# Performance work log

Hardware: AMD Instinct MI355X
Metric: run time of the kernel (lower is better)

## Reference

```python
import jax, jax.numpy as jnp
import numpy as np

GRID_SIZE = 64
THRESHOLD = 1.0
SIGMA = 1.5
K_SHARP = 2.0


def _gaussian_kernel(sigma):
    ksize = max(int(4 * sigma) | 1, 3)
    x = jnp.arange(ksize, dtype=jnp.float32) - ksize // 2
    g1d = jnp.exp(-x ** 2 / (2.0 * sigma ** 2))
    g2d = g1d[None, :] * g1d[:, None]
    g2d = g2d / g2d.sum()
    return g2d[None, None]  # (1,1,k,k) OIHW


def setup_inputs() -> dict:
    key = jax.random.key(0)
    k1, k2, k3, k4 = jax.random.split(key, 4)
    B, V, P, N, MAXP = 4, 512, 8192, 2000, 8
    positions = jax.random.uniform(k1, (B, V, 2), dtype=jnp.float32) * 2.0 - 1.0
    pin_offsets = jax.random.normal(k2, (P, 2), dtype=jnp.float32) * 0.05
    net_to_pin = jax.random.randint(k3, (N, MAXP), 0, P, dtype=jnp.int32)
    pin_to_macro = jax.random.randint(k4, (P,), 0, V, dtype=jnp.int32)
    return {"positions": positions, "pin_offsets": pin_offsets,
            "net_to_pin": net_to_pin, "pin_to_macro": pin_to_macro}


def reference(positions, pin_offsets, net_to_pin, pin_to_macro):
    B = positions.shape[0]
    M = GRID_SIZE
    num_nets = net_to_pin.shape[0]

    # pin positions: (B, P, 2) -- no rotation (rotation_onehot=None branch)
    pin_pos = positions[:, pin_to_macro, :] + pin_offsets[None]

    # per-net bounding boxes over valid pins
    valid = net_to_pin >= 0                                  # (N, maxp)
    safe_idx = jnp.maximum(net_to_pin, 0)
    net_pin_pos = pin_pos[:, safe_idx, :]                    # (B, N, maxp, 2)
    mask = valid[None, :, :, None]
    bbox_max = jnp.max(jnp.where(mask, net_pin_pos, -1e9), axis=2)  # (B, N, 2)
    bbox_min = jnp.min(jnp.where(mask, net_pin_pos, 1e9), axis=2)

    # to grid coordinates
    bbox_max_g = (bbox_max + 1.0) * 0.5 * (M - 1)
    bbox_min_g = (bbox_min + 1.0) * 0.5 * (M - 1)

    # soft rectangular indicators on the MxM grid
    gx = jnp.arange(M, dtype=jnp.float32)
    grid_x, grid_y = jnp.meshgrid(gx, gx, indexing="xy")     # (M, M)
    grid_x = grid_x[None, None]                               # (1,1,M,M)
    grid_y = grid_y[None, None]
    x_min = bbox_min_g[..., 0][..., None, None]               # (B,N,1,1)
    x_max = bbox_max_g[..., 0][..., None, None]
    y_min = bbox_min_g[..., 1][..., None, None]
    y_max = bbox_max_g[..., 1][..., None, None]

    in_x = jax.nn.sigmoid(K_SHARP * (grid_x - x_min + 0.5)) * \
           jax.nn.sigmoid(K_SHARP * (x_max - grid_x + 0.5))
    in_y = jax.nn.sigmoid(K_SHARP * (grid_y - y_min + 0.5)) * \
           jax.nn.sigmoid(K_SHARP * (y_max - grid_y + 0.5))
    indicator = in_x * in_y                                    # (B,N,M,M)

    bbox_size = jnp.maximum((x_max - x_min + 1.0) * (y_max - y_min + 1.0), 1.0)
    rudy = jnp.sum(indicator / bbox_size, axis=1, keepdims=True)  # (B,1,M,M)

    # gaussian smoothing (SAME padding)
    kernel = _gaussian_kernel(SIGMA)
    pad = kernel.shape[-1] // 2
    rudy_smooth = jax.lax.conv_general_dilated(
        rudy, kernel, window_strides=(1, 1),
        padding=((pad, pad), (pad, pad)),
        dimension_numbers=("NCHW", "OIHW", "NCHW"))

    overflow = jax.nn.relu(rudy_smooth - THRESHOLD)
    penalty = jnp.sum(overflow ** 2, axis=(1, 2, 3))           # (B,)
    return penalty, rudy_smooth
```

## Files before the change

kernel.cpp:

```cpp
#include <hip/hip_runtime.h>

#define GRID   64
#define CELLS  (GRID * GRID)
#define BATCH  4
#define NV     512
#define NNET   2000
#define MAXPIN 8
#define NB     32
#define NPART_MAX 63

__device__ __forceinline__ float sigmoidf_fast(float z) {
    return 1.0f / (1.0f + __expf(-z));
}

__global__ __launch_bounds__(256)
void rudy_partial_kernel(const float* __restrict__ positions,
                         const float* __restrict__ pin_offsets,
                         const int*   __restrict__ net_to_pin,
                         const int*   __restrict__ pin_to_macro,
                         float* __restrict__ partial,
                         int subs) {
    const int pb = blockIdx.x;
    const int b  = blockIdx.y;
    const int t  = threadIdx.x;

    __shared__ float s_inx[NB][GRID];
    __shared__ float s_iny[NB][GRID];
    __shared__ float s_xmin[NB], s_xmax[NB], s_ymin[NB], s_ymax[NB], s_inv[NB];

    const int lane = t & 63;
    const int w    = t >> 6;

    float acc[16];
    #pragma unroll
    for (int k = 0; k < 16; ++k) acc[k] = 0.0f;

    const int base = pb * subs * NB;

    for (int sub = 0; sub < subs; ++sub) {
        const int n0 = base + sub * NB;

        {
            const int nl = t >> 3;
            const int j  = t & 7;
            const int n  = n0 + nl;
            int pi = (n < NNET) ? net_to_pin[n * MAXPIN + j] : -1;
            int sp = pi > 0 ? pi : 0;
            int v  = pin_to_macro[sp];
            float px = positions[(b * NV + v) * 2 + 0] + pin_offsets[sp * 2 + 0];
            float py = positions[(b * NV + v) * 2 + 1] + pin_offsets[sp * 2 + 1];
            bool valid = pi >= 0;
            float xmx = valid ? px : -1e9f;
            float xmn = valid ? px :  1e9f;
            float ymx = valid ? py : -1e9f;
            float ymn = valid ? py :  1e9f;
            #pragma unroll
            for (int off = 1; off < 8; off <<= 1) {
                xmx = fmaxf(xmx, __shfl_xor(xmx, off, 64));
                xmn = fminf(xmn, __shfl_xor(xmn, off, 64));
                ymx = fmaxf(ymx, __shfl_xor(ymx, off, 64));
                ymn = fminf(ymn, __shfl_xor(ymn, off, 64));
            }
            if (j == 0) {
                float xming = (xmn + 1.0f) * 31.5f;
                float xmaxg = (xmx + 1.0f) * 31.5f;
                float yming = (ymn + 1.0f) * 31.5f;
                float ymaxg = (ymx + 1.0f) * 31.5f;
                float size = fmaxf((xmaxg - xming + 1.0f) * (ymaxg - yming + 1.0f), 1.0f);
                s_xmin[nl] = xming; s_xmax[nl] = xmaxg;
                s_ymin[nl] = yming; s_ymax[nl] = ymaxg;
                s_inv[nl]  = 1.0f / size;
            }
        }
        __syncthreads();

        #pragma unroll
        for (int i = 0; i < 16; ++i) {
            int vv    = i * 256 + t;
            int n     = vv >> 7;
            int rem   = vv & 127;
            int which = rem >> 6;
            int coord = rem & 63;
            float c  = (float)coord;
            float lo = which ? s_ymin[n] : s_xmin[n];
            float hi = which ? s_ymax[n] : s_xmax[n];
            float val = sigmoidf_fast(2.0f * (c - lo + 0.5f)) *
                        sigmoidf_fast(2.0f * (hi - c + 0.5f));
            if (which) s_iny[n][coord] = val;
            else       s_inx[n][coord] = val * s_inv[n];
        }
        __syncthreads();

        for (int n = 0; n < NB; ++n) {
            float xv = s_inx[n][lane];
            const float4* iny4 = (const float4*)&s_iny[n][w * 16];
            #pragma unroll
            for (int k4 = 0; k4 < 4; ++k4) {
                float4 yv = iny4[k4];
                acc[k4 * 4 + 0] += yv.x * xv;
                acc[k4 * 4 + 1] += yv.y * xv;
                acc[k4 * 4 + 2] += yv.z * xv;
                acc[k4 * 4 + 3] += yv.w * xv;
            }
        }
    }

    float* dst = partial + ((size_t)b * gridDim.x + pb) * CELLS;
    #pragma unroll
    for (int k = 0; k < 16; ++k)
        dst[(w * 16 + k) * GRID + lane] = acc[k];
}

__global__ __launch_bounds__(1024)
void reduce_smooth_kernel(const float* __restrict__ partial,
                          float* __restrict__ out_penalty,
                          float* __restrict__ out_smooth,
                          int npart) {
    const int b = blockIdx.x;
    const int t = threadIdx.x;

    __shared__ float tile[CELLS];
    __shared__ float tmp [CELLS];
    __shared__ float red [16];

    float g[7];
    {
        float s = 0.0f;
        #pragma unroll
        for (int i = 0; i < 7; ++i) {
            float d = (float)(i - 3);
            g[i] = expf(-d * d / 4.5f);
            s += g[i];
        }
        float inv = 1.0f / s;
        #pragma unroll
        for (int i = 0; i < 7; ++i) g[i] *= inv;
    }

    const float4* src = (const float4*)(partial + (size_t)b * npart * CELLS);
    float4 a = {0.0f, 0.0f, 0.0f, 0.0f};
    #pragma unroll 4
    for (int p = 0; p < npart; ++p) {
        float4 v = src[p * (CELLS / 4) + t];
        a.x += v.x; a.y += v.y; a.z += v.z; a.w += v.w;
    }
    ((float4*)tile)[t] = a;
    __syncthreads();

    #pragma unroll
    for (int i = 0; i < 4; ++i) {
        int c = i * 1024 + t;
        int y = c >> 6, x = c & 63;
        float s = 0.0f;
        #pragma unroll
        for (int d = -3; d <= 3; ++d) {
            int xx = x + d;
            if (xx >= 0 && xx < GRID) s += g[d + 3] * tile[y * GRID + xx];
        }
        tmp[c] = s;
    }
    __syncthreads();

    float local = 0.0f;
    #pragma unroll
    for (int i = 0; i < 4; ++i) {
        int c = i * 1024 + t;
        int y = c >> 6, x = c & 63;
        float s = 0.0f;
        #pragma unroll
        for (int d = -3; d <= 3; ++d) {
            int yy = y + d;
            if (yy >= 0 && yy < GRID) s += g[d + 3] * tmp[yy * GRID + x];
        }
        out_smooth[b * CELLS + c] = s;
        float ov = s - 1.0f;
        ov = ov > 0.0f ? ov : 0.0f;
        local += ov * ov;
    }

    #pragma unroll
    for (int off = 32; off > 0; off >>= 1) local += __shfl_down(local, off, 64);
    if ((t & 63) == 0) red[t >> 6] = local;
    __syncthreads();
    if (t == 0) {
        float s = 0.0f;
        #pragma unroll
        for (int i = 0; i < 16; ++i) s += red[i];
        out_penalty[b] = s;
    }
}

extern "C" void kernel_launch(void* const* d_in, const int* in_sizes, int n_in,
                              void* d_out, int out_size, void* d_ws, size_t ws_size,
                              hipStream_t stream) {
    const float* positions    = (const float*)d_in[0];
    const float* pin_offsets  = (const float*)d_in[1];
    const int*   net_to_pin   = (const int*)d_in[2];
    const int*   pin_to_macro = (const int*)d_in[3];
    float* out     = (float*)d_out;
    float* partial = (float*)d_ws;

    int npart = (int)(ws_size / ((size_t)BATCH * CELLS * sizeof(float)));
    if (npart > NPART_MAX) npart = NPART_MAX;
    if (npart < 1) npart = 1;
    int nets_per_block = (NNET + npart - 1) / npart;
    int subs = (nets_per_block + NB - 1) / NB;

    rudy_partial_kernel<<<dim3(npart, BATCH), 256, 0, stream>>>(
        positions, pin_offsets, net_to_pin, pin_to_macro, partial, subs);
    reduce_smooth_kernel<<<BATCH, 1024, 0, stream>>>(partial, out, out + BATCH, npart);
}
```

Measured before the change: 82.23 us.

## Split reduce/smooth across row bands and widen partial kernel to 512 threads

The partial kernel now uses 512 threads per block and handles exactly one 32-net chunk per block (63 blocks x 32 = 2016 nets), so the sub-loop and the workspace-derived partition count are gone. The reduce/smooth stage is split across 8 row bands per batch with halo rows, so 32 blocks work instead of 4. The penalty is accumulated with atomicAdd into a slot zeroed by the first kernel. The aim is to spread the reduction of 63 partial grids over more CUs. It assumes the workspace holds 63 partials and recomputes halo rows of the sums.

```diff
diff --git a/kernel.cpp b/kernel.cpp
--- a/kernel.cpp
+++ b/kernel.cpp
@@ -7,121 +7,121 @@
 #define NNET   2000
 #define MAXPIN 8
 #define NB     32
-#define NPART_MAX 63
-
-__device__ __forceinline__ float sigmoidf_fast(float z) {
-    return 1.0f / (1.0f + __expf(-z));
-}
-
-__global__ __launch_bounds__(256)
+#define NPART  63
+
+__device__ __forceinline__ float sig2(float a, float b) {
+    float e1 = __expf(-a);
+    float e2 = __expf(-b);
+    return 1.0f / ((1.0f + e1) * (1.0f + e2));
+}
+
+__global__ __launch_bounds__(512)
 void rudy_partial_kernel(const float* __restrict__ positions,
                          const float* __restrict__ pin_offsets,
                          const int*   __restrict__ net_to_pin,
                          const int*   __restrict__ pin_to_macro,
                          float* __restrict__ partial,
-                         int subs) {
+                         float* __restrict__ out_penalty) {
     const int pb = blockIdx.x;
     const int b  = blockIdx.y;
     const int t  = threadIdx.x;
 
+    if (pb == 0 && t == 0) out_penalty[b] = 0.0f;
+
     __shared__ float s_inx[NB][GRID];
     __shared__ float s_iny[NB][GRID];
     __shared__ float s_xmin[NB], s_xmax[NB], s_ymin[NB], s_ymax[NB], s_inv[NB];
 
+    const int n0 = pb * NB;
+
+    if (t < 256) {
+        const int nl = t >> 3;
+        const int j  = t & 7;
+        const int n  = n0 + nl;
+        int pi = (n < NNET) ? net_to_pin[n * MAXPIN + j] : -1;
+        int sp = pi > 0 ? pi : 0;
+        int v  = pin_to_macro[sp];
+        float px = positions[(b * NV + v) * 2 + 0] + pin_offsets[sp * 2 + 0];
+        float py = positions[(b * NV + v) * 2 + 1] + pin_offsets[sp * 2 + 1];
+        bool valid = pi >= 0;
+        float xmx = valid ? px : -1e9f;
+        float xmn = valid ? px :  1e9f;
+        float ymx = valid ? py : -1e9f;
+        float ymn = valid ? py :  1e9f;
+        #pragma unroll
+        for (int off = 1; off < 8; off <<= 1) {
+            xmx = fmaxf(xmx, __shfl_xor(xmx, off, 64));
+            xmn = fminf(xmn, __shfl_xor(xmn, off, 64));
+            ymx = fmaxf(ymx, __shfl_xor(ymx, off, 64));
+            ymn = fminf(ymn, __shfl_xor(ymn, off, 64));
+        }
+        if (j == 0) {
+            float xming = (xmn + 1.0f) * 31.5f;
+            float xmaxg = (xmx + 1.0f) * 31.5f;
+            float yming = (ymn + 1.0f) * 31.5f;
+            float ymaxg = (ymx + 1.0f) * 31.5f;
+            float size = fmaxf((xmaxg - xming + 1.0f) * (ymaxg - yming + 1.0f), 1.0f);
+            s_xmin[nl] = xming; s_xmax[nl] = xmaxg;
+            s_ymin[nl] = yming; s_ymax[nl] = ymaxg;
+            s_inv[nl]  = 1.0f / size;
+        }
+    }
+    __syncthreads();
+
+    #pragma unroll
+    for (int i = 0; i < 8; ++i) {
+        int vv    = i * 512 + t;
+        int n     = vv >> 7;
+        int rem   = vv & 127;
+        int which = rem >> 6;
+        int coord = rem & 63;
+        float c  = (float)coord;
+        float lo = which ? s_ymin[n] : s_xmin[n];
+        float hi = which ? s_ymax[n] : s_xmax[n];
+        float val = sig2(2.0f * (c - lo + 0.5f), 2.0f * (hi - c + 0.5f));
+        if (which) s_iny[n][coord] = val;
+        else       s_inx[n][coord] = val * s_inv[n];
+    }
+    __syncthreads();
+
     const int lane = t & 63;
     const int w    = t >> 6;
-
-    float acc[16];
-    #pragma unroll
-    for (int k = 0; k < 16; ++k) acc[k] = 0.0f;
-
-    const int base = pb * subs * NB;
-
-    for (int sub = 0; sub < subs; ++sub) {
-        const int n0 = base + sub * NB;
-
-        {
-            const int nl = t >> 3;
-            const int j  = t & 7;
-            const int n  = n0 + nl;
-            int pi = (n < NNET) ? net_to_pin[n * MAXPIN + j] : -1;
-            int sp = pi > 0 ? pi : 0;
-            int v  = pin_to_macro[sp];
-            float px = positions[(b * NV + v) * 2 + 0] + pin_offsets[sp * 2 + 0];
-            float py = positions[(b * NV + v) * 2 + 1] + pin_offsets[sp * 2 + 1];
-            bool valid = pi >= 0;
-            float xmx = valid ? px : -1e9f;
-            float xmn = valid ? px :  1e9f;
-            float ymx = valid ? py : -1e9f;
-            float ymn = valid ? py :  1e9f;
-            #pragma unroll
-            for (int off = 1; off < 8; off <<= 1) {
-                xmx = fmaxf(xmx, __shfl_xor(xmx, off, 64));
-                xmn = fminf(xmn, __shfl_xor(xmn, off, 64));
-                ymx = fmaxf(ymx, __shfl_xor(ymx, off, 64));
-                ymn = fminf(ymn, __shfl_xor(ymn, off, 64));
-            }
-            if (j == 0) {
-                float xming = (xmn + 1.0f) * 31.5f;
-                float xmaxg = (xmx + 1.0f) * 31.5f;
-                float yming = (ymn + 1.0f) * 31.5f;
-                float ymaxg = (ymx + 1.0f) * 31.5f;
-                float size = fmaxf((xmaxg - xming + 1.0f) * (ymaxg - yming + 1.0f), 1.0f);
-                s_xmin[nl] = xming; s_xmax[nl] = xmaxg;
-                s_ymin[nl] = yming; s_ymax[nl] = ymaxg;
-                s_inv[nl]  = 1.0f / size;
-            }
-        }
-        __syncthreads();
-
-        #pragma unroll
-        for (int i = 0; i < 16; ++i) {
-            int vv    = i * 256 + t;
-            int n     = vv >> 7;
-            int rem   = vv & 127;
-            int which = rem >> 6;
-            int coord = rem & 63;
-            float c  = (float)coord;
-            float lo = which ? s_ymin[n] : s_xmin[n];
-            float hi = which ? s_ymax[n] : s_xmax[n];
-            float val = sigmoidf_fast(2.0f * (c - lo + 0.5f)) *
-                        sigmoidf_fast(2.0f * (hi - c + 0.5f));
-            if (which) s_iny[n][coord] = val;
-            else       s_inx[n][coord] = val * s_inv[n];
-        }
-        __syncthreads();
-
-        for (int n = 0; n < NB; ++n) {
-            float xv = s_inx[n][lane];
-            const float4* iny4 = (const float4*)&s_iny[n][w * 16];
-            #pragma unroll
-            for (int k4 = 0; k4 < 4; ++k4) {
-                float4 yv = iny4[k4];
-                acc[k4 * 4 + 0] += yv.x * xv;
-                acc[k4 * 4 + 1] += yv.y * xv;
-                acc[k4 * 4 + 2] += yv.z * xv;
-                acc[k4 * 4 + 3] += yv.w * xv;
-            }
-        }
-    }
-
-    float* dst = partial + ((size_t)b * gridDim.x + pb) * CELLS;
-    #pragma unroll
-    for (int k = 0; k < 16; ++k)
-        dst[(w * 16 + k) * GRID + lane] = acc[k];
-}
-
-__global__ __launch_bounds__(1024)
-void reduce_smooth_kernel(const float* __restrict__ partial,
-                          float* __restrict__ out_penalty,
-                          float* __restrict__ out_smooth,
-                          int npart) {
-    const int b = blockIdx.x;
+    float acc[8];
+    #pragma unroll
+    for (int k = 0; k < 8; ++k) acc[k] = 0.0f;
+
+    for (int n = 0; n < NB; ++n) {
+        float xv = s_inx[n][lane];
+        const float4* iny4 = (const float4*)&s_iny[n][w * 8];
+        #pragma unroll
+        for (int k4 = 0; k4 < 2; ++k4) {
+            float4 yv = iny4[k4];
+            acc[k4 * 4 + 0] += yv.x * xv;
+            acc[k4 * 4 + 1] += yv.y * xv;
+            acc[k4 * 4 + 2] += yv.z * xv;
+            acc[k4 * 4 + 3] += yv.w * xv;
+        }
+    }
+
+    float* dst = partial + ((size_t)b * NPART + pb) * CELLS;
+    #pragma unroll
+    for (int k = 0; k < 8; ++k)
+        dst[(w * 8 + k) * GRID + lane] = acc[k];
+}
+
+#define SROWS 14
+__global__ __launch_bounds__(256)
+void reduce_smooth_penalty_kernel(const float* __restrict__ partial,
+                                  float* __restrict__ out_penalty,
+                                  float* __restrict__ out_smooth) {
+    const int q = blockIdx.x;
+    const int b = blockIdx.y;
     const int t = threadIdx.x;
-
-    __shared__ float tile[CELLS];
-    __shared__ float tmp [CELLS];
-    __shared__ float red [16];
+    const int y0 = q * 8;
+
+    __shared__ float tile[SROWS][GRID];
+    __shared__ float tmp [SROWS][GRID];
+    __shared__ float red [4];
 
     float g[7];
     {
@@ -137,42 +137,60 @@
         for (int i = 0; i < 7; ++i) g[i] *= inv;
     }
 
-    const float4* src = (const float4*)(partial + (size_t)b * npart * CELLS);
-    float4 a = {0.0f, 0.0f, 0.0f, 0.0f};
-    #pragma unroll 4
-    for (int p = 0; p < npart; ++p) {
-        float4 v = src[p * (CELLS / 4) + t];
-        a.x += v.x; a.y += v.y; a.z += v.z; a.w += v.w;
-    }
-    ((float4*)tile)[t] = a;
-    __syncthreads();
-
-    #pragma unroll
-    for (int i = 0; i < 4; ++i) {
-        int c = i * 1024 + t;
-        int y = c >> 6, x = c & 63;
+    if (t < SROWS * 16) {
+        const int r  = t >> 4;
+        const int c4 = t & 15;
+        const int yy = y0 - 3 + r;
+        float4 a0 = {0,0,0,0}, a1 = {0,0,0,0}, a2 = {0,0,0,0}, a3 = {0,0,0,0};
+        if (yy >= 0 && yy < GRID) {
+            const float4* src = (const float4*)(partial + (size_t)b * NPART * CELLS)
+                                + (size_t)yy * 16 + c4;
+            int p = 0;
+            for (; p + 3 < NPART; p += 4) {
+                float4 v0 = src[(size_t)(p + 0) * (CELLS / 4)];
+                float4 v1 = src[(size_t)(p + 1) * (CELLS / 4)];
+                float4 v2 = src[(size_t)(p + 2) * (CELLS / 4)];
+                float4 v3 = src[(size_t)(p + 3) * (CELLS / 4)];
+                a0.x += v0.x; a0.y += v0.y; a0.z += v0.z; a0.w += v0.w;
+                a1.x += v1.x; a1.y += v1.y; a1.z += v1.z; a1.w += v1.w;
+                a2.x += v2.x; a2.y += v2.y; a2.z += v2.z; a2.w += v2.w;
+                a3.x += v3.x; a3.y += v3.y; a3.z += v3.z; a3.w += v3.w;
+            }
+            for (; p < NPART; ++p) {
+                float4 v0 = src[(size_t)p * (CELLS / 4)];
+                a0.x += v0.x; a0.y += v0.y; a0.z += v0.z; a0.w += v0.w;
+            }
+            a0.x += a1.x + a2.x + a3.x;
+            a0.y += a1.y + a2.y + a3.y;
+            a0.z += a1.z + a2.z + a3.z;
+            a0.w += a1.w + a2.w + a3.w;
+        }
+        ((float4*)&tile[r][0])[c4] = a0;
+    }
+    __syncthreads();
+
+    for (int i = t; i < SROWS * GRID; i += 256) {
+        int r = i >> 6, x = i & 63;
         float s = 0.0f;
         #pragma unroll
         for (int d = -3; d <= 3; ++d) {
             int xx = x + d;
-            if (xx >= 0 && xx < GRID) s += g[d + 3] * tile[y * GRID + xx];
-        }
-        tmp[c] = s;
+            if (xx >= 0 && xx < GRID) s += g[d + 3] * tile[r][xx];
+        }
+        tmp[r][x] = s;
     }
     __syncthreads();
 
     float local = 0.0f;
     #pragma unroll
-    for (int i = 0; i < 4; ++i) {
-        int c = i * 1024 + t;
-        int y = c >> 6, x = c & 63;
+    for (int i = 0; i < 2; ++i) {
+        int c = i * 256 + t;
+        int r = c >> 6, x = c & 63;
         float s = 0.0f;
         #pragma unroll
-        for (int d = -3; d <= 3; ++d) {
-            int yy = y + d;
-            if (yy >= 0 && yy < GRID) s += g[d + 3] * tmp[yy * GRID + x];
-        }
-        out_smooth[b * CELLS + c] = s;
+        for (int d = -3; d <= 3; ++d)
+            s += g[d + 3] * tmp[r + 3 + d][x];
+        out_smooth[b * CELLS + (y0 + r) * GRID + x] = s;
         float ov = s - 1.0f;
         ov = ov > 0.0f ? ov : 0.0f;
         local += ov * ov;
@@ -182,12 +200,8 @@
     for (int off = 32; off > 0; off >>= 1) local += __shfl_down(local, off, 64);
     if ((t & 63) == 0) red[t >> 6] = local;
     __syncthreads();
-    if (t == 0) {
-        float s = 0.0f;
-        #pragma unroll
-        for (int i = 0; i < 16; ++i) s += red[i];
-        out_penalty[b] = s;
-    }
+    if (t == 0)
+        atomicAdd(&out_penalty[b], red[0] + red[1] + red[2] + red[3]);
 }
 
 extern "C" void kernel_launch(void* const* d_in, const int* in_sizes, int n_in,
@@ -200,13 +214,8 @@
     float* out     = (float*)d_out;
     float* partial = (float*)d_ws;
 
-    int npart = (int)(ws_size / ((size_t)BATCH * CELLS * sizeof(float)));
-    if (npart > NPART_MAX) npart = NPART_MAX;
-    if (npart < 1) npart = 1;
-    int nets_per_block = (NNET + npart - 1) / npart;
-    int subs = (nets_per_block + NB - 1) / NB;
-
-    rudy_partial_kernel<<<dim3(npart, BATCH), 256, 0, stream>>>(
-        positions, pin_offsets, net_to_pin, pin_to_macro, partial, subs);
-    reduce_smooth_kernel<<<BATCH, 1024, 0, stream>>>(partial, out, out + BATCH, npart);
-}
+    rudy_partial_kernel<<<dim3(NPART, BATCH), 512, 0, stream>>>(
+        positions, pin_offsets, net_to_pin, pin_to_macro, partial, out);
+    reduce_smooth_penalty_kernel<<<dim3(8, BATCH), 256, 0, stream>>>(
+        partial, out, out + BATCH);
+}
```

After: 74.65 us. 9.2% less time.
